# Optimization experiments

Hardware: AMD Instinct MI355X
Metric: run time of the kernel (lower is better)

## Reference

```python
import jax, jax.numpy as jnp
import numpy as np

N = 50000      # nodes per graph
E = 800000     # directed edges per graph
D_IN, C1, C2, C3, K = 96, 64, 32, 16, 16  # K = tensor_neurons (Linear(16,16) forces 16)


def setup_inputs() -> dict:
    key = jax.random.key(0)
    ks = jax.random.split(key, 18)
    def w(k, shape, scale=0.1):
        return (jax.random.normal(k, shape, jnp.float32) * scale)
    return {
        "features_1": jax.random.normal(ks[0], (N, D_IN), jnp.float32),
        "features_2": jax.random.normal(ks[1], (N, D_IN), jnp.float32),
        "edges_1": jax.random.randint(ks[2], (2, E), 0, N),
        "edges_2": jax.random.randint(ks[3], (2, E), 0, N),
        # GCN layer params (PyG GCNConv: X @ W then normalized aggregation, then + b)
        "W1": w(ks[4], (D_IN, C1)), "b1": jnp.zeros((C1,), jnp.float32),
        "W2": w(ks[5], (C1, C2)),  "b2": jnp.zeros((C2,), jnp.float32),
        "W3": w(ks[6], (C2, C3)),  "b3": jnp.zeros((C3,), jnp.float32),
        # Attention pooling weight matrix [C3, C3]
        "Wa": w(ks[7], (C3, C3)),
        # Tensor network: bilinear tensor [C3, C3, K], block [K, 2*C3], bias [K]
        "Wt": w(ks[8], (C3, C3, K)),
        "Wb": w(ks[9], (K, 2 * C3)),
        "bt": w(ks[10], (K,)),
        # fully_connected_first Linear(16,16) and scoring Linear(16,1)
        "Wfc": w(ks[11], (K, 16)), "bfc": jnp.zeros((16,), jnp.float32),
        "Wsc": w(ks[12], (16, 1)), "bsc": jnp.zeros((1,), jnp.float32),
    }


def gcn_conv(x, src, dst, W, b):
    # PyG GCNConv with self-loops: D^-1/2 (A+I) D^-1/2 (X W) + b
    h = x @ W                                   # [N, C]
    ones = jnp.ones(src.shape[0], h.dtype)
    deg = jax.ops.segment_sum(ones, dst, num_segments=N) + 1.0   # in-degree + self loop
    dinv = jax.lax.rsqrt(deg)                   # [N]
    coef = dinv[src] * dinv[dst]                # [E]
    agg = jax.ops.segment_sum(h[src] * coef[:, None], dst, num_segments=N)
    return agg + h * (dinv * dinv)[:, None] + b  # self-loop term has norm dinv_i^2


def encode(x, edges, W1, b1, W2, b2, W3, b3):
    src, dst = edges[0], edges[1]
    x = jax.nn.relu(gcn_conv(x, src, dst, W1, b1))  # dropout is a no-op in eval mode
    x = jax.nn.relu(gcn_conv(x, src, dst, W2, b2))
    return gcn_conv(x, src, dst, W3, b3)


def attention_pool(x, Wa):
    # SimGNN AttentionModule: c = tanh(mean(x Wa)); s = sigmoid(x c); rep = x^T s
    c = jnp.tanh(jnp.mean(x @ Wa, axis=0))      # [C3]
    s = jax.nn.sigmoid(x @ c)                   # [N]
    return x.T @ s                              # [C3]


def reference(features_1, features_2, edges_1, edges_2,
              W1, b1, W2, b2, W3, b3, Wa, Wt, Wb, bt, Wfc, bfc, Wsc, bsc):
    h1 = encode(features_1, edges_1, W1, b1, W2, b2, W3, b3)
    h2 = encode(features_2, edges_2, W1, b1, W2, b2, W3, b3)
    e1 = attention_pool(h1, Wa)                 # [C3]
    e2 = attention_pool(h2, Wa)                 # [C3]
    # Tensor network scoring
    bilinear = jnp.einsum('i,ijk,j->k', e1, Wt, e2)        # [K]
    block = Wb @ jnp.concatenate([e1, e2])                 # [K]
    scores = jax.nn.relu(bilinear + block + bt)            # [K]
    scores = jnp.tanh(scores @ Wfc + bfc)                  # [16]
    score = jax.nn.sigmoid(scores @ Wsc + bsc)             # [1]
    return score
```

## Files before the change

### kernel.cpp

```cpp
#include <hip/hip_runtime.h>
#include <hip/hip_bf16.h>

#define TPB 256
#define SH 6
#define BW 64

typedef unsigned short u16;
typedef __attribute__((ext_vector_type(8))) __bf16 bf16x8;
typedef __attribute__((ext_vector_type(4))) float f32x4;

__device__ __forceinline__ u16 f_to_bf(float f) {
    unsigned u = __float_as_uint(f);
    return (u16)((u + 0x7fff + ((u >> 16) & 1)) >> 16);
}
__device__ __forceinline__ float4 bf4_to_f4(ushort4 v) {
    float4 r;
    r.x = __uint_as_float((unsigned)v.x << 16);
    r.y = __uint_as_float((unsigned)v.y << 16);
    r.z = __uint_as_float((unsigned)v.z << 16);
    r.w = __uint_as_float((unsigned)v.w << 16);
    return r;
}
__device__ __forceinline__ void facc(float4& a, float4 v) {
    a.x += v.x; a.y += v.y; a.z += v.z; a.w += v.w;
}
__device__ __forceinline__ float4 shfl_xor4(float4 v, int mask, int width) {
    v.x = __shfl_xor(v.x, mask, width);
    v.y = __shfl_xor(v.y, mask, width);
    v.z = __shfl_xor(v.z, mask, width);
    v.w = __shfl_xor(v.w, mask, width);
    return v;
}

template <int C>
__device__ __forceinline__ float4 gather_sum(const u16* __restrict__ HW,
                                             const int* __restrict__ col,
                                             int c0, int ps, int pe) {
    float4 a0 = make_float4(0.f, 0.f, 0.f, 0.f);
    float4 a1 = a0, a2 = a0, a3 = a0;
    int p = ps;
    for (; p + 8 <= pe; p += 8) {
        int j[8];
        ushort4 d[8];
#pragma unroll
        for (int k = 0; k < 8; k++) j[k] = col[p + k];
#pragma unroll
        for (int k = 0; k < 8; k++) d[k] = *(const ushort4*)&HW[(size_t)j[k] * C + c0];
        facc(a0, bf4_to_f4(d[0])); facc(a1, bf4_to_f4(d[1]));
        facc(a2, bf4_to_f4(d[2])); facc(a3, bf4_to_f4(d[3]));
        facc(a0, bf4_to_f4(d[4])); facc(a1, bf4_to_f4(d[5]));
        facc(a2, bf4_to_f4(d[6])); facc(a3, bf4_to_f4(d[7]));
    }
    if (p + 4 <= pe) {
        int j[4];
        ushort4 d[4];
#pragma unroll
        for (int k = 0; k < 4; k++) j[k] = col[p + k];
#pragma unroll
        for (int k = 0; k < 4; k++) d[k] = *(const ushort4*)&HW[(size_t)j[k] * C + c0];
        facc(a0, bf4_to_f4(d[0])); facc(a1, bf4_to_f4(d[1]));
        facc(a2, bf4_to_f4(d[2])); facc(a3, bf4_to_f4(d[3]));
        p += 4;
    }
    for (; p < pe; p++) {
        int j = col[p];
        facc(a0, bf4_to_f4(*(const ushort4*)&HW[(size_t)j * C + c0]));
    }
    facc(a0, a1); facc(a2, a3); facc(a0, a2);
    return a0;
}


__global__ void bucket_scatter_kernel(const int* __restrict__ e0, const int* __restrict__ e1,
                                      int E, int* __restrict__ bcur,
                                      int* __restrict__ ebuf0, int* __restrict__ ebuf1,
                                      int nbuk, int cap) {
    int g = blockIdx.y;
    const int* src = g ? e1 : e0;
    const int* dst = src + E;
    int* ebuf = g ? ebuf1 : ebuf0;
    int* bu = bcur + g * 1024;
    __shared__ int hist[1024];
    for (int t = threadIdx.x; t < 1024; t += TPB) hist[t] = 0;
    __syncthreads();
    int base = blockIdx.x * 4096;
    int pk[16], bk[16], rk[16];
#pragma unroll
    for (int k = 0; k < 16; k++) {
        int e = base + k * TPB + (int)threadIdx.x;
        bk[k] = -1;
        if (e < E) {
            int s = src[e], d = dst[e];
            int b = d >> SH;
            bk[k] = b;
            pk[k] = (s << SH) | (d & (BW - 1));
            rk[k] = atomicAdd(&hist[b], 1);
        }
    }
    __syncthreads();
    for (int t = threadIdx.x; t < nbuk; t += TPB) {
        int h = hist[t];
        hist[t] = h ? atomicAdd(&bu[t], h) : 0;
    }
    __syncthreads();
#pragma unroll
    for (int k = 0; k < 16; k++)
        if (bk[k] >= 0) {
            int pos = hist[bk[k]] + rk[k];
            if (pos < cap) ebuf[(size_t)bk[k] * cap + pos] = pk[k];
        }
}

__global__ void bucket_csr_kernel(const int* __restrict__ ebuf0, const int* __restrict__ ebuf1,
                                  const int* __restrict__ bcur, int n, int cap,
                                  int* __restrict__ soff0, int* __restrict__ soff1,
                                  int* __restrict__ eoff0, int* __restrict__ eoff1,
                                  float* __restrict__ dinv0, float* __restrict__ dinv1,
                                  int* __restrict__ col0, int* __restrict__ col1) {
    int g = blockIdx.y;
    int b = blockIdx.x;
    const int* ebuf = g ? ebuf1 : ebuf0;
    int* soff = g ? soff1 : soff0;
    int* eoff = g ? eoff1 : eoff0;
    float* dinv = g ? dinv1 : dinv0;
    int* col = g ? col1 : col0;
    __shared__ int h[BW], nb[BW], nrank[BW];
    int tid = threadIdx.x;
    if (tid < BW) h[tid] = 0;
    __syncthreads();
    int s = b * cap;
    int cnt = min(bcur[g * 1024 + b], cap);
    int e = s + cnt;
    for (int i = s + tid; i < e; i += TPB)
        atomicAdd(&h[ebuf[i] & (BW - 1)], 1);
    __syncthreads();
    if (tid < BW) {
        int v = h[tid];
        int x = v;
        for (int d = 1; d < BW; d <<= 1) {
            int u = __shfl_up(x, d, 64);
            if (tid >= d) x += u;
        }
        int base = s + x - v;
        nb[tid] = base;
        nrank[tid] = 0;
        int node = b * BW + tid;
        if (node < n) {
            soff[node] = base;
            eoff[node] = base + v;
            dinv[node] = rsqrtf((float)v + 1.0f);
        }
    }
    __syncthreads();
    for (int i = s + tid; i < e; i += TPB) {
        int p = ebuf[i];
        int lo = p & (BW - 1);
        int r = atomicAdd(&nrank[lo], 1);
        col[nb[lo] + r] = p >> SH;
    }
}


template <int CIN, int COUT>
__global__ void matmul_kernel(const float* __restrict__ X0, const float* __restrict__ X1,
                              const float* __restrict__ W,
                              const float* __restrict__ dinv0, const float* __restrict__ dinv1,
                              u16* __restrict__ Y0, u16* __restrict__ Y1, int n) {
    constexpr int CINP = CIN + 8;
    constexpr int NT = COUT / 16;
    constexpr int KT = CIN / 32;
    __shared__ u16 Xs[64 * CINP];
    __shared__ u16 Wt[COUT * CINP];

    int g = blockIdx.y;
    const float* X = g ? X1 : X0;
    const float* dinv = g ? dinv1 : dinv0;
    u16* Y = g ? Y1 : Y0;
    int nb0 = blockIdx.x * 64;

    for (int i = threadIdx.x; i < 64 * (CIN / 4); i += TPB) {
        int nn = i / (CIN / 4), kc = i % (CIN / 4);
        float4 v = make_float4(0.f, 0.f, 0.f, 0.f);
        if (nb0 + nn < n) v = *(const float4*)&X[(size_t)(nb0 + nn) * CIN + 4 * kc];
        ushort4 b;
        b.x = f_to_bf(v.x); b.y = f_to_bf(v.y); b.z = f_to_bf(v.z); b.w = f_to_bf(v.w);
        *(ushort4*)&Xs[nn * CINP + 4 * kc] = b;
    }
    for (int i = threadIdx.x; i < CIN * (COUT / 4); i += TPB) {
        int k = i / (COUT / 4), nc4 = i % (COUT / 4);
        float4 v = *(const float4*)&W[(size_t)k * COUT + 4 * nc4];
        Wt[(4 * nc4 + 0) * CINP + k] = f_to_bf(v.x);
        Wt[(4 * nc4 + 1) * CINP + k] = f_to_bf(v.y);
        Wt[(4 * nc4 + 2) * CINP + k] = f_to_bf(v.z);
        Wt[(4 * nc4 + 3) * CINP + k] = f_to_bf(v.w);
    }
    __syncthreads();

    int lane = threadIdx.x & 63;
    int w = threadIdx.x >> 6;
    int m = lane & 15;
    int quad = lane >> 4;

    f32x4 acc[NT];
#pragma unroll
    for (int t = 0; t < NT; t++) acc[t] = (f32x4){0.f, 0.f, 0.f, 0.f};
#pragma unroll
    for (int kt = 0; kt < KT; kt++) {
        int k0 = kt * 32 + quad * 8;
        bf16x8 a = *(const bf16x8*)&Xs[(w * 16 + m) * CINP + k0];
#pragma unroll
        for (int t = 0; t < NT; t++) {
            bf16x8 b = *(const bf16x8*)&Wt[(t * 16 + m) * CINP + k0];
            acc[t] = __builtin_amdgcn_mfma_f32_16x16x32_bf16(a, b, acc[t], 0, 0, 0);
        }
    }
#pragma unroll
    for (int r = 0; r < 4; r++) {
        int node = nb0 + w * 16 + quad * 4 + r;
        if (node < n) {
            float d = dinv[node];
#pragma unroll
            for (int t = 0; t < NT; t++)
                Y[(size_t)node * COUT + t * 16 + m] = f_to_bf(acc[t][r] * d);
        }
    }
}


template <int C, int SPLIT, int COUT2>
__global__ __launch_bounds__(TPB, 2)
void agg_mm_kernel(const u16* __restrict__ HW0, const u16* __restrict__ HW1,
                   const int* __restrict__ soff0, const int* __restrict__ soff1,
                   const int* __restrict__ eoff0, const int* __restrict__ eoff1,
                   const int* __restrict__ col0, const int* __restrict__ col1,
                   const float* __restrict__ dinv0, const float* __restrict__ dinv1,
                   const float* __restrict__ bias, const float* __restrict__ W2,
                   u16* __restrict__ Y0, u16* __restrict__ Y1, int n) {
    constexpr int CH = C / 4;
    constexpr int TPN = CH * SPLIT;
    constexpr int HS = C + 4;
    constexpr int OPT = 16 * COUT2 / TPB;
    __shared__ float Ws2[C * COUT2];
    __shared__ float Hs[16 * HS];

    int g = blockIdx.y;
    const u16* HW = g ? HW1 : HW0;
    const int* soff = g ? soff1 : soff0;
    const int* eoff = g ? eoff1 : eoff0;
    const int* col = g ? col1 : col0;
    const float* dinv = g ? dinv1 : dinv0;
    u16* Y = g ? Y1 : Y0;

    for (int i = threadIdx.x; i < C * COUT2 / 4; i += TPB)
        ((float4*)Ws2)[i] = ((const float4*)W2)[i];

    int tid = blockIdx.x * TPB + (int)threadIdx.x;
    int node = tid / TPN;
    int nl = threadIdx.x / TPN;
    int part = threadIdx.x % TPN;
    int sp = part / CH;
    int c0 = (part % CH) * 4;
    float4 o = make_float4(0.f, 0.f, 0.f, 0.f);
    if (node < n) {
        int s = soff[node], e = eoff[node];
        int len = e - s;
        int chunk = (len + SPLIT - 1) / SPLIT;
        int ps = s + sp * chunk;
        int pe = min(ps + chunk, e);
        float4 r = gather_sum<C>(HW, col, c0, ps, pe);
#pragma unroll
        for (int m = CH; m < TPN; m <<= 1) facc(r, shfl_xor4(r, m, TPN));
        if (sp == 0) {
            float di = dinv[node];
            float4 self = bf4_to_f4(*(const ushort4*)&HW[(size_t)node * C + c0]);
            float4 b4 = *(const float4*)&bias[c0];
            o.x = fmaxf(di * (r.x + self.x) + b4.x, 0.f);
            o.y = fmaxf(di * (r.y + self.y) + b4.y, 0.f);
            o.z = fmaxf(di * (r.z + self.z) + b4.z, 0.f);
            o.w = fmaxf(di * (r.w + self.w) + b4.w, 0.f);
        }
    }
    if (sp == 0) *(float4*)&Hs[nl * HS + c0] = o;
    __syncthreads();

    int nl2 = threadIdx.x >> 4;
    int p2 = threadIdx.x & 15;
    int onode = blockIdx.x * 16 + nl2;
    if (onode < n) {
        float d = dinv[onode];
        float acc[OPT];
#pragma unroll
        for (int j = 0; j < OPT; j++) acc[j] = 0.f;
#pragma unroll
        for (int k = 0; k < C; k++) {
            float h = Hs[nl2 * HS + k];
#pragma unroll
            for (int j = 0; j < OPT; j++)
                acc[j] += h * Ws2[k * COUT2 + p2 * OPT + j];
        }
        if constexpr (OPT == 2) {
            unsigned pack = (unsigned)f_to_bf(acc[0] * d) | ((unsigned)f_to_bf(acc[1] * d) << 16);
            *(unsigned*)&Y[(size_t)onode * COUT2 + p2 * 2] = pack;
        } else {
            Y[(size_t)onode * COUT2 + p2] = f_to_bf(acc[0] * d);
        }
    }
}

__global__ __launch_bounds__(TPB, 2)
void agg16_kernel(const u16* __restrict__ HW0, const u16* __restrict__ HW1,
                  const int* __restrict__ soff0, const int* __restrict__ soff1,
                  const int* __restrict__ eoff0, const int* __restrict__ eoff1,
                  const int* __restrict__ col0, const int* __restrict__ col1,
                  const float* __restrict__ dinv0, const float* __restrict__ dinv1,
                  const float* __restrict__ bias,
                  float* __restrict__ out0, float* __restrict__ out1,
                  float* __restrict__ pcol, int n) {
    int g = blockIdx.y;
    const u16* HW = g ? HW1 : HW0;
    const int* soff = g ? soff1 : soff0;
    const int* eoff = g ? eoff1 : eoff0;
    const int* col = g ? col1 : col0;
    const float* dinv = g ? dinv1 : dinv0;
    float* outp = g ? out1 : out0;
    int tid = blockIdx.x * blockDim.x + threadIdx.x;
    int node = tid / 16;
    int part = tid % 16;
    int sp = part / 4;
    int c0 = (part % 4) * 4;
    float4 o = make_float4(0.f, 0.f, 0.f, 0.f);
    if (node < n) {
        int s = soff[node], e = eoff[node];
        int len = e - s;
        int chunk = (len + 3) / 4;
        int ps = s + sp * chunk;
        int pe = min(ps + chunk, e);
        float4 r = gather_sum<16>(HW, col, c0, ps, pe);
        facc(r, shfl_xor4(r, 4, 16));
        facc(r, shfl_xor4(r, 8, 16));
        if (sp == 0) {
            float di = dinv[node];
            float4 self = bf4_to_f4(*(const ushort4*)&HW[(size_t)node * 16 + c0]);
            float4 b4 = *(const float4*)&bias[c0];
            o.x = di * (r.x + self.x) + b4.x;
            o.y = di * (r.y + self.y) + b4.y;
            o.z = di * (r.z + self.z) + b4.z;
            o.w = di * (r.w + self.w) + b4.w;
            *(float4*)&outp[(size_t)node * 16 + c0] = o;
        }
    }
    __shared__ float4 sd[TPB];
    sd[threadIdx.x] = (node < n && sp == 0) ? o : make_float4(0.f, 0.f, 0.f, 0.f);
    __syncthreads();
    if (threadIdx.x < 64) {
        float4 a = sd[threadIdx.x];
        facc(a, sd[threadIdx.x + 64]);
        facc(a, sd[threadIdx.x + 128]);
        facc(a, sd[threadIdx.x + 192]);
        sd[threadIdx.x] = a;
    }
    __syncthreads();
    if (threadIdx.x < 16) {
        float4 a = sd[threadIdx.x];
        facc(a, sd[threadIdx.x + 16]);
        facc(a, sd[threadIdx.x + 32]);
        facc(a, sd[threadIdx.x + 48]);
        sd[threadIdx.x] = a;
    }
    __syncthreads();
    if (threadIdx.x < 4)
        *(float4*)&pcol[((size_t)g * gridDim.x + blockIdx.x) * 16 + threadIdx.x * 4] = sd[threadIdx.x];
}


__global__ void cvec_kernel(const float* __restrict__ pcol, int nb16, float n_inv,
                            const float* __restrict__ Wa, float* __restrict__ cvec) {
    int g = blockIdx.x;
    const float4* p4 = (const float4*)(pcol + (size_t)g * nb16 * 16);
    __shared__ float4 sd[TPB];
    __shared__ float cs[16];
    int c4 = threadIdx.x & 3;
    int row = threadIdx.x >> 2;
    float4 acc = make_float4(0.f, 0.f, 0.f, 0.f);
    for (int r = row; r < nb16; r += 64) facc(acc, p4[(size_t)r * 4 + c4]);
    sd[threadIdx.x] = acc;
    __syncthreads();
    if (threadIdx.x < 64) {
        float4 a = sd[threadIdx.x];
        facc(a, sd[threadIdx.x + 64]);
        facc(a, sd[threadIdx.x + 128]);
        facc(a, sd[threadIdx.x + 192]);
        sd[threadIdx.x] = a;
    }
    __syncthreads();
    if (threadIdx.x < 16) {
        float4 a = sd[threadIdx.x];
        facc(a, sd[threadIdx.x + 16]);
        facc(a, sd[threadIdx.x + 32]);
        facc(a, sd[threadIdx.x + 48]);
        sd[threadIdx.x] = a;
    }
    __syncthreads();
    if (threadIdx.x < 4) {
        float4 a = sd[threadIdx.x];
        facc(a, sd[threadIdx.x + 4]);
        facc(a, sd[threadIdx.x + 8]);
        facc(a, sd[threadIdx.x + 12]);
        cs[threadIdx.x * 4 + 0] = a.x * n_inv;
        cs[threadIdx.x * 4 + 1] = a.y * n_inv;
        cs[threadIdx.x * 4 + 2] = a.z * n_inv;
        cs[threadIdx.x * 4 + 3] = a.w * n_inv;
    }
    __syncthreads();
    if (threadIdx.x < 16) {
        float acc2 = 0.f;
#pragma unroll
        for (int i = 0; i < 16; i++) acc2 += cs[i] * Wa[i * 16 + threadIdx.x];
        cvec[g * 16 + threadIdx.x] = tanhf(acc2);
    }
}


__global__ void pool_kernel(const float* __restrict__ H0, const float* __restrict__ H1, int n,
                            const float* __restrict__ cvec, float* __restrict__ ppool) {
    int g = blockIdx.y;
    const float* H = g ? H1 : H0;
    int c = threadIdx.x & 15;
    float cv = cvec[g * 16 + c];
    int w = (blockIdx.x * blockDim.x + threadIdx.x) / 16;
    int stride = (gridDim.x * blockDim.x) / 16;
    float acc = 0.f;
    for (int node = w; node < n; node += stride) {
        float x = H[(size_t)node * 16 + c];
        float p = x * cv;
        p += __shfl_xor(p, 1, 16);
        p += __shfl_xor(p, 2, 16);
        p += __shfl_xor(p, 4, 16);
        p += __shfl_xor(p, 8, 16);
        float s = 1.f / (1.f + __expf(-p));
        acc += s * x;
    }
    __shared__ float sdata[TPB];
    sdata[threadIdx.x] = acc;
    __syncthreads();
    if (threadIdx.x < 16) {
        float s = 0.f;
        for (int t = threadIdx.x; t < TPB; t += 16) s += sdata[t];
        ppool[((size_t)g * gridDim.x + blockIdx.x) * 16 + threadIdx.x] = s;
    }
}


__global__ void final_kernel(const float* __restrict__ ppool, int nbp,
                             const float* __restrict__ Wt, const float* __restrict__ Wb,
                             const float* __restrict__ bt, const float* __restrict__ Wfc,
                             const float* __restrict__ bfc, const float* __restrict__ Wsc,
                             const float* __restrict__ bsc, float* __restrict__ out) {
    __shared__ float4 sd4[TPB];
    __shared__ float rep[32], part[TPB], scores[16], tvec[16];
    int t = threadIdx.x;
    {
        const float4* p4 = (const float4*)ppool;
        int g = t >> 7;
        int r0 = (t >> 2) & 31;
        int c4 = t & 3;
        float4 acc = make_float4(0.f, 0.f, 0.f, 0.f);
        for (int r = r0; r < nbp; r += 32)
            facc(acc, p4[((size_t)g * nbp + r) * 4 + c4]);
        sd4[t] = acc;
        __syncthreads();
        for (int st = 16; st >= 1; st >>= 1) {
            if (r0 < st) facc(sd4[t], sd4[t + st * 4]);
            __syncthreads();
        }
        if (r0 == 0) {
            float4 a = sd4[t];
            rep[g * 16 + c4 * 4 + 0] = a.x;
            rep[g * 16 + c4 * 4 + 1] = a.y;
            rep[g * 16 + c4 * 4 + 2] = a.z;
            rep[g * 16 + c4 * 4 + 3] = a.w;
        }
        __syncthreads();
    }
    {
        int p = t >> 4, tt = t & 15;
        float b = 0.f;
#pragma unroll
        for (int q = 0; q < 16; q++)
            b += rep[q] * Wt[(q * 16 + p) * 16 + tt];
        part[t] = b * rep[16 + p];
    }
    __syncthreads();
    if (t < 16) {
        float bil = 0.f;
#pragma unroll
        for (int p = 0; p < 16; p++) bil += part[p * 16 + t];
        float blk = 0.f;
#pragma unroll
        for (int m = 0; m < 16; m++)
            blk += Wb[t * 32 + m] * rep[m] + Wb[t * 32 + 16 + m] * rep[16 + m];
        scores[t] = fmaxf(bil + blk + bt[t], 0.f);
    }
    __syncthreads();
    if (t < 16) {
        float acc = bfc[t];
#pragma unroll
        for (int k = 0; k < 16; k++) acc += scores[k] * Wfc[k * 16 + t];
        tvec[t] = tanhf(acc);
    }
    __syncthreads();
    if (t == 0) {
        float acc = bsc[0];
#pragma unroll
        for (int j = 0; j < 16; j++) acc += tvec[j] * Wsc[j];
        out[0] = 1.f / (1.f + __expf(-acc));
    }
}


extern "C" void kernel_launch(void* const* d_in, const int* in_sizes, int n_in,
                              void* d_out, int out_size, void* d_ws, size_t ws_size,
                              hipStream_t stream) {
    const float* X1 = (const float*)d_in[0];
    const float* X2 = (const float*)d_in[1];
    const int* edges1 = (const int*)d_in[2];
    const int* edges2 = (const int*)d_in[3];
    const float* W1 = (const float*)d_in[4];
    const float* b1 = (const float*)d_in[5];
    const float* W2 = (const float*)d_in[6];
    const float* b2 = (const float*)d_in[7];
    const float* W3 = (const float*)d_in[8];
    const float* b3 = (const float*)d_in[9];
    const float* Wa = (const float*)d_in[10];
    const float* Wt = (const float*)d_in[11];
    const float* Wb = (const float*)d_in[12];
    const float* bt = (const float*)d_in[13];
    const float* Wfc = (const float*)d_in[14];
    const float* bfc = (const float*)d_in[15];
    const float* Wsc = (const float*)d_in[16];
    const float* bsc = (const float*)d_in[17];
    float* out = (float*)d_out;

    const int N = in_sizes[0] / 96;
    const int E = in_sizes[2] / 2;
    const int NBUK = (N + BW - 1) / BW;
    int cap = ((2 * (E / NBUK)) + 255) & ~255;
    if (cap < 256) cap = 256;

    char* ws = (char*)d_ws;
    size_t o = 0;
    auto alloc = [&](size_t bytes) {
        void* p = ws + o;
        o += (bytes + 255) & ~(size_t)255;
        return p;
    };
    int* bcur = (int*)alloc((size_t)2 * 1024 * 4);
    int* soff0 = (int*)alloc((size_t)N * 4);
    int* soff1 = (int*)alloc((size_t)N * 4);
    int* eoff0 = (int*)alloc((size_t)N * 4);
    int* eoff1 = (int*)alloc((size_t)N * 4);
    int* col0 = (int*)alloc((size_t)NBUK * cap * 4);
    int* col1 = (int*)alloc((size_t)NBUK * cap * 4);
    int* ebuf0 = (int*)alloc((size_t)NBUK * cap * 4);
    int* ebuf1 = (int*)alloc((size_t)NBUK * cap * 4);
    float* dinv0 = (float*)alloc((size_t)N * 4);
    float* dinv1 = (float*)alloc((size_t)N * 4);
    u16* hwbA0 = (u16*)alloc((size_t)N * 64 * 2);
    u16* hwbA1 = (u16*)alloc((size_t)N * 64 * 2);
    u16* hwbB0 = (u16*)alloc((size_t)N * 32 * 2);
    u16* hwbB1 = (u16*)alloc((size_t)N * 32 * 2);
    u16* hwbC0 = (u16*)alloc((size_t)N * 16 * 2);
    u16* hwbC1 = (u16*)alloc((size_t)N * 16 * 2);
    float* H30 = (float*)alloc((size_t)N * 16 * 4);
    float* H31 = (float*)alloc((size_t)N * 16 * 4);

    const int gB2 = (E + 4095) / 4096;
    const int g16 = ((size_t)N * 16 + TPB - 1) / TPB;
    const int gMM = (N + 63) / 64;
    const int gPool = 256;

    float* pcol = (float*)alloc((size_t)2 * g16 * 16 * 4);
    float* cvecArr = (float*)alloc(32 * 4);
    float* ppool = (float*)alloc((size_t)2 * gPool * 16 * 4);

    hipMemsetAsync(bcur, 0, (size_t)2 * 1024 * 4, stream);

    bucket_scatter_kernel<<<dim3(gB2, 2), TPB, 0, stream>>>(edges1, edges2, E, bcur,
                                                            ebuf0, ebuf1, NBUK, cap);
    bucket_csr_kernel<<<dim3(NBUK, 2), TPB, 0, stream>>>(ebuf0, ebuf1, bcur, N, cap,
                                                         soff0, soff1, eoff0, eoff1,
                                                         dinv0, dinv1, col0, col1);

    matmul_kernel<96, 64><<<dim3(gMM, 2), TPB, 0, stream>>>(X1, X2, W1, dinv0, dinv1, hwbA0, hwbA1, N);
    agg_mm_kernel<64, 1, 32><<<dim3(g16, 2), TPB, 0, stream>>>(
        hwbA0, hwbA1, soff0, soff1, eoff0, eoff1, col0, col1, dinv0, dinv1, b1, W2, hwbB0, hwbB1, N);
    agg_mm_kernel<32, 2, 16><<<dim3(g16, 2), TPB, 0, stream>>>(
        hwbB0, hwbB1, soff0, soff1, eoff0, eoff1, col0, col1, dinv0, dinv1, b2, W3, hwbC0, hwbC1, N);
    agg16_kernel<<<dim3(g16, 2), TPB, 0, stream>>>(
        hwbC0, hwbC1, soff0, soff1, eoff0, eoff1, col0, col1, dinv0, dinv1, b3, H30, H31, pcol, N);

    cvec_kernel<<<2, TPB, 0, stream>>>(pcol, g16, 1.0f / (float)N, Wa, cvecArr);
    pool_kernel<<<dim3(gPool, 2), TPB, 0, stream>>>(H30, H31, N, cvecArr, ppool);
    final_kernel<<<1, 256, 0, stream>>>(ppool, gPool, Wt, Wb, bt, Wfc, bfc, Wsc, bsc, out);
}
```

Baseline: 262.6 us.

## Use MFMA bf16 for fused aggregation matmul and interleave graph blocks

Replaces the scalar FMA loop that multiplies the aggregated 16-node tile by W2/W3 with bf16 MFMA 16x16x32 instructions, storing the aggregated activations and the transposed weights as bf16 in shared memory. It also replaces the 2D grid with a 1D swizzled grid that interleaves blocks of the two graphs in groups of four, to balance work across CUs. The MFMA path adds a bf16 rounding of intermediate activations and weights, which may change accuracy slightly. Weight staging now converts per element instead of using float4 copies.

After: 261.0 us. About the same (-0.6%).

```diff
diff --git a/kernel.cpp b/kernel.cpp
--- a/kernel.cpp
+++ b/kernel.cpp
@@ -30,6 +30,14 @@
     v.z = __shfl_xor(v.z, mask, width);
     v.w = __shfl_xor(v.w, mask, width);
     return v;
+}
+
+__device__ __forceinline__ bool swz_block(int nblk, int& g, int& bx) {
+    int blk = blockIdx.x;
+    int j = blk & 7;
+    g = j >> 2;
+    bx = (blk >> 3) * 4 + (j & 3);
+    return bx < nblk;
 }
 
 template <int C>
@@ -235,15 +243,17 @@
                    const int* __restrict__ col0, const int* __restrict__ col1,
                    const float* __restrict__ dinv0, const float* __restrict__ dinv1,
                    const float* __restrict__ bias, const float* __restrict__ W2,
-                   u16* __restrict__ Y0, u16* __restrict__ Y1, int n) {
+                   u16* __restrict__ Y0, u16* __restrict__ Y1, int n, int nblk) {
     constexpr int CH = C / 4;
     constexpr int TPN = CH * SPLIT;
-    constexpr int HS = C + 4;
-    constexpr int OPT = 16 * COUT2 / TPB;
-    __shared__ float Ws2[C * COUT2];
-    __shared__ float Hs[16 * HS];
-
-    int g = blockIdx.y;
+    constexpr int CP = C + 8;
+    constexpr int NT2 = COUT2 / 16;
+    constexpr int KT2 = C / 32;
+    __shared__ __align__(16) u16 HsB[16 * CP];
+    __shared__ __align__(16) u16 WtB[COUT2 * CP];
+
+    int g, bx;
+    if (!swz_block(nblk, g, bx)) return;
     const u16* HW = g ? HW1 : HW0;
     const int* soff = g ? soff1 : soff0;
     const int* eoff = g ? eoff1 : eoff0;
@@ -251,10 +261,12 @@
     const float* dinv = g ? dinv1 : dinv0;
     u16* Y = g ? Y1 : Y0;
 
-    for (int i = threadIdx.x; i < C * COUT2 / 4; i += TPB)
-        ((float4*)Ws2)[i] = ((const float4*)W2)[i];
-
-    int tid = blockIdx.x * TPB + (int)threadIdx.x;
+    for (int idx = threadIdx.x; idx < C * COUT2; idx += TPB) {
+        int k = idx / COUT2, nc = idx % COUT2;
+        WtB[nc * CP + k] = f_to_bf(W2[idx]);
+    }
+
+    int tid = bx * TPB + (int)threadIdx.x;
     int node = tid / TPN;
     int nl = threadIdx.x / TPN;
     int part = threadIdx.x % TPN;
@@ -280,29 +292,32 @@
             o.w = fmaxf(di * (r.w + self.w) + b4.w, 0.f);
         }
     }
-    if (sp == 0) *(float4*)&Hs[nl * HS + c0] = o;
-    __syncthreads();
-
-    int nl2 = threadIdx.x >> 4;
-    int p2 = threadIdx.x & 15;
-    int onode = blockIdx.x * 16 + nl2;
-    if (onode < n) {
-        float d = dinv[onode];
-        float acc[OPT];
-#pragma unroll
-        for (int j = 0; j < OPT; j++) acc[j] = 0.f;
-#pragma unroll
-        for (int k = 0; k < C; k++) {
-            float h = Hs[nl2 * HS + k];
-#pragma unroll
-            for (int j = 0; j < OPT; j++)
-                acc[j] += h * Ws2[k * COUT2 + p2 * OPT + j];
-        }
-        if constexpr (OPT == 2) {
-            unsigned pack = (unsigned)f_to_bf(acc[0] * d) | ((unsigned)f_to_bf(acc[1] * d) << 16);
-            *(unsigned*)&Y[(size_t)onode * COUT2 + p2 * 2] = pack;
-        } else {
-            Y[(size_t)onode * COUT2 + p2] = f_to_bf(acc[0] * d);
+    if (sp == 0) {
+        ushort4 hb;
+        hb.x = f_to_bf(o.x); hb.y = f_to_bf(o.y); hb.z = f_to_bf(o.z); hb.w = f_to_bf(o.w);
+        *(ushort4*)&HsB[nl * CP + c0] = hb;
+    }
+    __syncthreads();
+
+    int lane = threadIdx.x & 63;
+    int w = threadIdx.x >> 6;
+    if (w < NT2) {
+        int m = lane & 15;
+        int quad = lane >> 4;
+        f32x4 acc = (f32x4){0.f, 0.f, 0.f, 0.f};
+#pragma unroll
+        for (int kt = 0; kt < KT2; kt++) {
+            int k0 = kt * 32 + quad * 8;
+            bf16x8 a = *(const bf16x8*)&HsB[m * CP + k0];
+            bf16x8 b = *(const bf16x8*)&WtB[(w * 16 + m) * CP + k0];
+            acc = __builtin_amdgcn_mfma_f32_16x16x32_bf16(a, b, acc, 0, 0, 0);
+        }
+        int base16 = bx * 16;
+#pragma unroll
+        for (int r = 0; r < 4; r++) {
+            int onode = base16 + quad * 4 + r;
+            if (onode < n)
+                Y[(size_t)onode * COUT2 + w * 16 + m] = f_to_bf(acc[r] * dinv[onode]);
         }
     }
 }
@@ -315,15 +330,16 @@
                   const float* __restrict__ dinv0, const float* __restrict__ dinv1,
                   const float* __restrict__ bias,
                   float* __restrict__ out0, float* __restrict__ out1,
-                  float* __restrict__ pcol, int n) {
-    int g = blockIdx.y;
+                  float* __restrict__ pcol, int n, int nblk) {
+    int g, bx;
+    if (!swz_block(nblk, g, bx)) return;
     const u16* HW = g ? HW1 : HW0;
     const int* soff = g ? soff1 : soff0;
     const int* eoff = g ? eoff1 : eoff0;
     const int* col = g ? col1 : col0;
     const float* dinv = g ? dinv1 : dinv0;
     float* outp = g ? out1 : out0;
-    int tid = blockIdx.x * blockDim.x + threadIdx.x;
+    int tid = bx * TPB + (int)threadIdx.x;
     int node = tid / 16;
     int part = tid % 16;
     int sp = part / 4;
@@ -369,7 +385,7 @@
     }
     __syncthreads();
     if (threadIdx.x < 4)
-        *(float4*)&pcol[((size_t)g * gridDim.x + blockIdx.x) * 16 + threadIdx.x * 4] = sd[threadIdx.x];
+        *(float4*)&pcol[((size_t)g * nblk + bx) * 16 + threadIdx.x * 4] = sd[threadIdx.x];
 }
 
 
@@ -576,6 +592,7 @@
 
     const int gB2 = (E + 4095) / 4096;
     const int g16 = ((size_t)N * 16 + TPB - 1) / TPB;
+    const int gSwz = 8 * ((g16 + 3) / 4);
     const int gMM = (N + 63) / 64;
     const int gPool = 256;
 
@@ -592,12 +609,15 @@
                                                          dinv0, dinv1, col0, col1);
 
     matmul_kernel<96, 64><<<dim3(gMM, 2), TPB, 0, stream>>>(X1, X2, W1, dinv0, dinv1, hwbA0, hwbA1, N);
-    agg_mm_kernel<64, 1, 32><<<dim3(g16, 2), TPB, 0, stream>>>(
-        hwbA0, hwbA1, soff0, soff1, eoff0, eoff1, col0, col1, dinv0, dinv1, b1, W2, hwbB0, hwbB1, N);
-    agg_mm_kernel<32, 2, 16><<<dim3(g16, 2), TPB, 0, stream>>>(
-        hwbB0, hwbB1, soff0, soff1, eoff0, eoff1, col0, col1, dinv0, dinv1, b2, W3, hwbC0, hwbC1, N);
-    agg16_kernel<<<dim3(g16, 2), TPB, 0, stream>>>(
-        hwbC0, hwbC1, soff0, soff1, eoff0, eoff1, col0, col1, dinv0, dinv1, b3, H30, H31, pcol, N);
+    agg_mm_kernel<64, 1, 32><<<gSwz, TPB, 0, stream>>>(
+        hwbA0, hwbA1, soff0, soff1, eoff0, eoff1, col0, col1, dinv0, dinv1, b1, W2,
+        hwbB0, hwbB1, N, g16);
+    agg_mm_kernel<32, 2, 16><<<gSwz, TPB, 0, stream>>>(
+        hwbB0, hwbB1, soff0, soff1, eoff0, eoff1, col0, col1, dinv0, dinv1, b2, W3,
+        hwbC0, hwbC1, N, g16);
+    agg16_kernel<<<gSwz, TPB, 0, stream>>>(
+        hwbC0, hwbC1, soff0, soff1, eoff0, eoff1, col0, col1, dinv0, dinv1, b3,
+        H30, H31, pcol, N, g16);
 
     cvec_kernel<<<2, TPB, 0, stream>>>(pcol, g16, 1.0f / (float)N, Wa, cvecArr);
     pool_kernel<<<dim3(gPool, 2), TPB, 0, stream>>>(H30, H31, N, cvecArr, ppool);
```
